# Kernel optimization log

Hardware: AMD Instinct MI355X
Metric: run time of the kernel (lower is better)

Reference implementation:

```python
import jax, jax.numpy as jnp
import numpy as np

B, SEQ, C, H, L = 2, 512, 768, 12, 6
OBS = ACT = GOAL = 64
MAXEP = 1000
D = C // H
T3 = 3 * SEQ  # stacked (z, state, action) tokens per timestep


def _ln(x, g, b):
    m = jnp.mean(x, -1, keepdims=True)
    v = jnp.mean((x - m) ** 2, -1, keepdims=True)
    return (x - m) * jax.lax.rsqrt(v + 1e-5) * g + b


def setup_inputs() -> dict:
    key = jax.random.key(0)
    it = iter(jax.random.split(key, 64))
    nrm = lambda shape, s=0.02: jax.random.normal(next(it), shape, jnp.float32) * s
    z = lambda *s: jnp.zeros(s, jnp.float32)
    o = lambda *s: jnp.ones(s, jnp.float32)
    return dict(
        states=jax.random.normal(next(it), (B, SEQ, OBS), jnp.float32),
        actions=jax.random.normal(next(it), (B, SEQ, ACT), jnp.float32),
        goals=jax.random.normal(next(it), (B, 1, GOAL), jnp.float32),
        traj_mask=jnp.ones((B, SEQ), bool),
        timesteps=jax.random.randint(next(it), (B, SEQ), 0, MAXEP),
        W_s=nrm((OBS, C)), b_s=z(C),
        W_a=nrm((ACT, C)), b_a=z(C),
        W_g=nrm((GOAL, C)), b_g=z(C),
        E_t=nrm((MAXEP, C)),
        ln0_g=o(C), ln0_b=z(C),
        Wq=nrm((L, C, C)), bq=z(L, C),
        Wk=nrm((L, C, C)), bk=z(L, C),
        Wv=nrm((L, C, C)), bv=z(L, C),
        Wp=nrm((L, C, C)), bp=z(L, C),
        ln1_g=o(L, C), ln1_b=z(L, C),
        W1=nrm((L, C, 4 * C)), b1=z(L, 4 * C),
        W2=nrm((L, 4 * C, C)), b2=z(L, C),
        ln2_g=o(L, C), ln2_b=z(L, C),
        W_ps=nrm((C, OBS)), b_ps=z(OBS),
        W_pa=nrm((C, ACT)), b_pa=z(ACT),
    )


def _forward(states, actions, goals, timesteps,
             W_s, b_s, W_a, b_a, W_g, b_g, E_t, ln0_g, ln0_b,
             Wq, bq, Wk, bk, Wv, bv, Wp, bp, ln1_g, ln1_b,
             W1, b1, W2, b2, ln2_g, ln2_b, W_ps, b_ps, W_pa, b_pa):
    te = E_t[timesteps]  # [B,SEQ,C] time embeddings (use_pe_as_timestep path)
    s_emb = states @ W_s + b_s + te
    a_emb = actions @ W_a + b_a + te
    g = jnp.broadcast_to(goals, (goals.shape[0], SEQ, goals.shape[2]))
    z_emb = g @ W_g + b_g + te  # GOAL_CONDITION path
    # interleave (z, s, a) per timestep -> [B, 3*SEQ, C]
    x = jnp.stack((z_emb, s_emb, a_emb), axis=2).reshape(states.shape[0], T3, C)
    x = _ln(x, ln0_g, ln0_b)
    mask = jnp.tril(jnp.ones((T3, T3), bool))
    scale = 1.0 / np.sqrt(D)
    for l in range(L):
        q = (x @ Wq[l] + bq[l]).reshape(-1, T3, H, D)
        k = (x @ Wk[l] + bk[l]).reshape(-1, T3, H, D)
        v = (x @ Wv[l] + bv[l]).reshape(-1, T3, H, D)
        sc = jnp.einsum('bqhd,bkhd->bhqk', q, k) * scale
        sc = jnp.where(mask, sc, -jnp.inf)
        w = jax.nn.softmax(sc, axis=-1)
        att = jnp.einsum('bhqk,bkhd->bqhd', w, v).reshape(-1, T3, C)
        x = x + att @ Wp[l] + bp[l]
        x = _ln(x, ln1_g[l], ln1_b[l])
        h = jax.nn.gelu(x @ W1[l] + b1[l], approximate=False)
        x = x + h @ W2[l] + b2[l]
        x = _ln(x, ln2_g[l], ln2_b[l])
    x = x.reshape(-1, SEQ, 3, C)
    state_preds = x[:, :, 2] @ W_ps + b_ps     # read off action-token positions
    action_preds = jnp.tanh(x[:, :, 1] @ W_pa + b_pa)  # state-token positions
    return jnp.stack((state_preds, action_preds))  # [2,B,SEQ,64]


def reference(states, actions, goals, traj_mask, timesteps,
              W_s, b_s, W_a, b_a, W_g, b_g, E_t, ln0_g, ln0_b,
              Wq, bq, Wk, bk, Wv, bv, Wp, bp, ln1_g, ln1_b,
              W1, b1, W2, b2, ln2_g, ln2_b, W_ps, b_ps, W_pa, b_pa):
    del traj_mask  # unused on the GOAL_CONDITION path
    return _forward(states, actions, goals, timesteps,
                    W_s, b_s, W_a, b_a, W_g, b_g, E_t, ln0_g, ln0_b,
                    Wq, bq, Wk, bk, Wv, bv, Wp, bp, ln1_g, ln1_b,
                    W1, b1, W2, b2, ln2_g, ln2_b, W_ps, b_ps, W_pa, b_pa)
```

## Files before the change

kernel.cpp:

```cpp
#include <hip/hip_runtime.h>

#define SEQ 512
#define T3 1536
#define CDIM 768
#define NH 12
#define HD 64
#define NL 6

typedef __attribute__((ext_vector_type(8))) short bh8;
typedef __attribute__((ext_vector_type(4))) short s4;
typedef __attribute__((ext_vector_type(4))) float f4;

__device__ inline short f2bf(float f) {
    union { float f; unsigned u; } x; x.f = f;
    unsigned r = x.u + 0x7FFFu + ((x.u >> 16) & 1u);
    return (short)(r >> 16);
}

__device__ inline void gload16(const short* g, const short* l) {
    __builtin_amdgcn_global_load_lds(
        (const __attribute__((address_space(1))) unsigned int*)g,
        (__attribute__((address_space(3))) unsigned int*)l, 16, 0, 0);
}

__device__ inline float block_sum(float v, volatile float* red, int tid) {
    #pragma unroll
    for (int off = 32; off > 0; off >>= 1) v += __shfl_down(v, off, 64);
    __syncthreads();
    if ((tid & 63) == 0) red[tid >> 6] = v;
    __syncthreads();
    return red[0] + red[1] + red[2] + red[3];
}

__global__ __launch_bounds__(256) void conv64_k(
        const float* __restrict__ Wq, const float* __restrict__ Wk,
        const float* __restrict__ Wv, const float* __restrict__ Wp,
        const float* __restrict__ W1, const float* __restrict__ W2,
        short* __restrict__ dst, int l) {
    int r = blockIdx.x;
    const float* src; short* d; int K, N, tk, tn;
    if (r < 576) {
        int mat = r / 144, t = r - mat * 144;
        tk = t / 12; tn = t % 12; K = 768; N = 768;
        const float* srcs[4] = {Wq, Wk, Wv, Wp};
        src = srcs[mat] + (size_t)l * 589824;
        d = dst + mat * 589824;
    } else if (r < 1152) {
        int t = r - 576; tk = t / 48; tn = t % 48; K = 768; N = 3072;
        src = W1 + (size_t)l * 2359296; d = dst + 2359296;
    } else {
        int t = r - 1152; tk = t / 12; tn = t % 12; K = 3072; N = 768;
        src = W2 + (size_t)l * 2359296; d = dst + 4718592;
    }
    int k0 = tk * 64, n0 = tn * 64;
    __shared__ float t2[64][65];
    int tid = threadIdx.x;
    int rk = tid >> 4, cn4 = (tid & 15) * 4;
    #pragma unroll
    for (int p = 0; p < 4; ++p) {
        f4 v = *(const f4*)(src + (size_t)(k0 + p * 16 + rk) * N + n0 + cn4);
        #pragma unroll
        for (int j = 0; j < 4; ++j) t2[cn4 + j][p * 16 + rk] = v[j];
    }
    __syncthreads();
    int n = tid >> 2, kb = (tid & 3) * 16;
    bh8 o0, o1;
    #pragma unroll
    for (int j = 0; j < 8; ++j) o0[j] = f2bf(t2[n][kb + j]);
    #pragma unroll
    for (int j = 0; j < 8; ++j) o1[j] = f2bf(t2[n][kb + 8 + j]);
    short* wp = d + (size_t)(n0 + n) * K + k0 + kb;
    *(bh8*)wp = o0;
    *(bh8*)(wp + 8) = o1;
}

__global__ __launch_bounds__(256) void embed_ln0_k(
        const float* __restrict__ states, const float* __restrict__ actions,
        const float* __restrict__ goals, const int* __restrict__ timesteps,
        const float* __restrict__ W_s, const float* __restrict__ b_s,
        const float* __restrict__ W_a, const float* __restrict__ b_a,
        const float* __restrict__ W_g, const float* __restrict__ b_g,
        const float* __restrict__ E_t, const float* __restrict__ g0,
        const float* __restrict__ bb0, float* __restrict__ x, short* __restrict__ xb) {
    int row = blockIdx.x;
    int b = row / T3, t3 = row - b * T3;
    int t = t3 / 3, kind = t3 - t * 3;
    __shared__ float inv[64];
    __shared__ float xr[CDIM];
    __shared__ float red[4];
    int tid = threadIdx.x;
    const float* src; const float* W; const float* bias;
    if (kind == 0)      { src = goals + b * 64;                       W = W_g; bias = b_g; }
    else if (kind == 1) { src = states + ((size_t)b * SEQ + t) * 64;  W = W_s; bias = b_s; }
    else                { src = actions + ((size_t)b * SEQ + t) * 64; W = W_a; bias = b_a; }
    if (tid < 64) inv[tid] = src[tid];
    __syncthreads();
    int ts = timesteps[b * SEQ + t];
    for (int c = tid; c < CDIM; c += 256) {
        float acc = bias[c] + E_t[(size_t)ts * CDIM + c];
        #pragma unroll 8
        for (int kk = 0; kk < 64; ++kk) acc += inv[kk] * W[kk * CDIM + c];
        xr[c] = acc;
    }
    __syncthreads();
    float v0 = xr[tid], v1 = xr[tid + 256], v2 = xr[tid + 512];
    float mean = block_sum(v0 + v1 + v2, red, tid) * (1.f / CDIM);
    float d0 = v0 - mean, d1 = v1 - mean, d2 = v2 - mean;
    float var = block_sum(d0 * d0 + d1 * d1 + d2 * d2, red, tid) * (1.f / CDIM);
    float rs = rsqrtf(var + 1e-5f);
    float* w = x + (size_t)row * CDIM;
    short* wb = xb + (size_t)row * CDIM;
    float o0 = d0 * rs * g0[tid]       + bb0[tid];
    float o1 = d1 * rs * g0[tid + 256] + bb0[tid + 256];
    float o2 = d2 * rs * g0[tid + 512] + bb0[tid + 512];
    w[tid] = o0; w[tid + 256] = o1; w[tid + 512] = o2;
    wb[tid] = f2bf(o0); wb[tid + 256] = f2bf(o1); wb[tid + 512] = f2bf(o2);
}

__global__ __launch_bounds__(256) void ln_k(const float* __restrict__ in, float* __restrict__ outp,
                                            short* __restrict__ outb,
                                            const float* __restrict__ g, const float* __restrict__ bb) {
    int row = blockIdx.x, tid = threadIdx.x;
    __shared__ float red[4];
    const float* r = in + (size_t)row * CDIM;
    float v0 = r[tid], v1 = r[tid + 256], v2 = r[tid + 512];
    float mean = block_sum(v0 + v1 + v2, red, tid) * (1.f / CDIM);
    float d0 = v0 - mean, d1 = v1 - mean, d2 = v2 - mean;
    float var = block_sum(d0 * d0 + d1 * d1 + d2 * d2, red, tid) * (1.f / CDIM);
    float rs = rsqrtf(var + 1e-5f);
    float* w = outp + (size_t)row * CDIM;
    short* wb = outb + (size_t)row * CDIM;
    float o0 = d0 * rs * g[tid]       + bb[tid];
    float o1 = d1 * rs * g[tid + 256] + bb[tid + 256];
    float o2 = d2 * rs * g[tid + 512] + bb[tid + 512];
    w[tid] = o0; w[tid + 256] = o1; w[tid + 512] = o2;
    wb[tid] = f2bf(o0); wb[tid + 256] = f2bf(o1); wb[tid + 512] = f2bf(o2);
}

template<int BM, int EPI>
__global__ __launch_bounds__(256) void gemm3_k(
        const short* __restrict__ A, const short* __restrict__ B0,
        const short* __restrict__ B1, const short* __restrict__ B2,
        const float* __restrict__ bias0, const float* __restrict__ bias1,
        const float* __restrict__ bias2, const float* __restrict__ res,
        float* __restrict__ outF, short* __restrict__ outQ,
        short* __restrict__ outK, short* __restrict__ outV,
        int N, int K) {
    const short* Bw = B0; const float* bias = bias0; short* outB = outQ;
    int zid = 0;
    if (EPI == 0) {
        zid = blockIdx.z;
        if (zid == 1) { Bw = B1; bias = bias1; outB = outK; }
        else if (zid == 2) { Bw = B2; bias = bias2; outB = outV; }
    }
    __shared__ short As[BM * 64];
    __shared__ short Bs[128 * 64];
    int tid = threadIdx.x, lane = tid & 63, wave = tid >> 6;
    int wm = wave >> 1, wn = wave & 1, lr = lane & 15, lg = lane >> 4;
    int bm = blockIdx.y * BM, bn = blockIdx.x * 128;
    int rl = lane >> 3, ch = (lane & 7) ^ rl;
    constexpr int MI = BM / 32;
    f4 acc[MI][4] = {};
    for (int k0 = 0; k0 < K; k0 += 64) {
        #pragma unroll
        for (int j = 0; j < BM / 32; ++j)
            gload16(A + (size_t)(bm + wave * (BM / 4) + j * 8 + rl) * K + k0 + ch * 8,
                    As + (wave * (BM / 4) + j * 8) * 64);
        #pragma unroll
        for (int j = 0; j < 4; ++j)
            gload16(Bw + (size_t)(bn + wave * 32 + j * 8 + rl) * K + k0 + ch * 8,
                    Bs + (wave * 32 + j * 8) * 64);
        __syncthreads();
        bh8 af[MI][2], bf[4][2];
        #pragma unroll
        for (int mi = 0; mi < MI; ++mi)
        #pragma unroll
        for (int kk = 0; kk < 2; ++kk) {
            int m = wm * (BM / 2) + mi * 16 + lr;
            af[mi][kk] = *(const bh8*)(As + m * 64 + (((kk * 4 + lg) ^ (lr & 7)) * 8));
        }
        #pragma unroll
        for (int ni = 0; ni < 4; ++ni)
        #pragma unroll
        for (int kk = 0; kk < 2; ++kk) {
            int n = wn * 64 + ni * 16 + lr;
            bf[ni][kk] = *(const bh8*)(Bs + n * 64 + (((kk * 4 + lg) ^ (lr & 7)) * 8));
        }
        #pragma unroll
        for (int kk = 0; kk < 2; ++kk)
        #pragma unroll
        for (int mi = 0; mi < MI; ++mi)
        #pragma unroll
        for (int ni = 0; ni < 4; ++ni)
            acc[mi][ni] = __builtin_amdgcn_mfma_f32_16x16x32_bf16(af[mi][kk], bf[ni][kk], acc[mi][ni], 0, 0, 0);
        __syncthreads();
    }
    #pragma unroll
    for (int mi = 0; mi < MI; ++mi)
    #pragma unroll
    for (int ni = 0; ni < 4; ++ni)
    #pragma unroll
    for (int i = 0; i < 4; ++i) {
        int row = bm + wm * (BM / 2) + mi * 16 + lg * 4 + i;
        int col = bn + wn * 64 + ni * 16 + lr;
        float vv = acc[mi][ni][i] + bias[col];
        if (EPI == 0) {
            int b = row / T3, t = row - b * T3;
            int h = col >> 6, d = col & 63;
            if (zid == 2) outB[((size_t)(b * NH + h) * 64 + d) * T3 + t] = f2bf(vv);
            else          outB[((((size_t)b * NH + h) * T3 + t) << 6) + d] = f2bf(vv);
        } else if (EPI == 1) {
            outF[(size_t)row * N + col] = vv + res[(size_t)row * N + col];
        } else {
            float gl = 0.5f * vv * (1.0f + erff(vv * 0.70710678118f));
            outQ[(size_t)row * N + col] = f2bf(gl);
        }
    }
}

__global__ __launch_bounds__(256) void attn_k(const short* __restrict__ q, const short* __restrict__ k,
                                              const short* __restrict__ vt, short* __restrict__ att) {
    int idx = blockIdx.x;
    int qt = 23 - (idx / 24);
    int bh = idx % 24;
    int b = bh / NH, h = bh - b * NH;
    const short* qb = q  + (size_t)bh * T3 * HD;
    const short* kb = k  + (size_t)bh * T3 * HD;
    const short* vb = vt + (size_t)bh * HD * T3;
    __shared__ short Ks[2][4096];
    __shared__ short Vs[2][4096];
    __shared__ short Pl[4][16][72];
    int tid = threadIdx.x, lane = tid & 63, wave = tid >> 6;
    int lr = lane & 15, lg = lane >> 4;
    int rl = lane >> 3, ch = (lane & 7) ^ rl;
    int qrow0 = qt * 64 + wave * 16;
    bh8 aq0 = *(const bh8*)(qb + (size_t)(qrow0 + lr) * HD + lg * 8);
    bh8 aq1 = *(const bh8*)(qb + (size_t)(qrow0 + lr) * HD + 32 + lg * 8);
    f4 o[4] = {};
    float lsum[4] = {0.f, 0.f, 0.f, 0.f};

    auto STAGE = [&](int kt2, int buf) {
        const short* kb2 = kb + (size_t)kt2 * 64 * HD;
        #pragma unroll
        for (int j = 0; j < 2; ++j)
            gload16(kb2 + (wave * 16 + j * 8 + rl) * HD + ch * 8,
                    &Ks[buf][(wave * 16 + j * 8) * 64]);
        const short* vb2 = vb + kt2 * 64;
        #pragma unroll
        for (int j = 0; j < 2; ++j)
            gload16(vb2 + (size_t)(wave * 16 + j * 8 + rl) * T3 + ch * 8,
                    &Vs[buf][(wave * 16 + j * 8) * 64]);
    };

    STAGE(0, 0);
    int cur = 0;
    for (int kt = 0; kt <= qt; ++kt) {
        if (kt < qt) {
            STAGE(kt + 1, cur ^ 1);
            asm volatile("s_waitcnt vmcnt(4)" ::: "memory");
        } else {
            asm volatile("s_waitcnt vmcnt(0)" ::: "memory");
        }
        __builtin_amdgcn_s_barrier();
        __builtin_amdgcn_sched_barrier(0);
        const short* Kb = &Ks[cur][0];
        const short* Vb = &Vs[cur][0];
        f4 s[4];
        #pragma unroll
        for (int nf = 0; nf < 4; ++nf) {
            int tok = nf * 16 + lr;
            bh8 bk0 = *(const bh8*)(Kb + tok * 64 + ((lg ^ (lr & 7)) * 8));
            bh8 bk1 = *(const bh8*)(Kb + tok * 64 + (((4 + lg) ^ (lr & 7)) * 8));
            f4 t = {};
            t = __builtin_amdgcn_mfma_f32_16x16x32_bf16(aq0, bk0, t, 0, 0, 0);
            t = __builtin_amdgcn_mfma_f32_16x16x32_bf16(aq1, bk1, t, 0, 0, 0);
            s[nf] = t;
        }
        #pragma unroll
        for (int nf = 0; nf < 4; ++nf)
        #pragma unroll
        for (int i = 0; i < 4; ++i) {
            float p = __expf(s[nf][i] * 0.125f);
            if (kt == qt && (nf * 16 + lr) > (wave * 16 + lg * 4 + i)) p = 0.f;
            lsum[i] += p;
            Pl[wave][lg * 4 + i][nf * 16 + lr] = f2bf(p);
        }
        bh8 ap0 = *(const bh8*)&Pl[wave][lr][lg * 8];
        bh8 ap1 = *(const bh8*)&Pl[wave][lr][32 + lg * 8];
        #pragma unroll
        for (int nf = 0; nf < 4; ++nf) {
            int d = nf * 16 + lr;
            bh8 bv0 = *(const bh8*)(Vb + d * 64 + ((lg ^ (lr & 7)) * 8));
            bh8 bv1 = *(const bh8*)(Vb + d * 64 + (((4 + lg) ^ (lr & 7)) * 8));
            o[nf] = __builtin_amdgcn_mfma_f32_16x16x32_bf16(ap0, bv0, o[nf], 0, 0, 0);
            o[nf] = __builtin_amdgcn_mfma_f32_16x16x32_bf16(ap1, bv1, o[nf], 0, 0, 0);
        }
        __builtin_amdgcn_sched_barrier(0);
        __builtin_amdgcn_s_barrier();
        cur ^= 1;
    }
    float linv[4];
    #pragma unroll
    for (int i = 0; i < 4; ++i) {
        float l = lsum[i];
        #pragma unroll
        for (int off = 1; off < 16; off <<= 1) l += __shfl_xor(l, off, 16);
        linv[i] = 1.f / l;
    }
    #pragma unroll
    for (int nf = 0; nf < 4; ++nf)
    #pragma unroll
    for (int i = 0; i < 4; ++i) {
        int qrow = qrow0 + lg * 4 + i;
        att[((size_t)b * T3 + qrow) * CDIM + h * 64 + nf * 16 + lr] = f2bf(o[nf][i] * linv[i]);
    }
}

__global__ __launch_bounds__(64) void head_k(const float* __restrict__ x,
                                             const float* __restrict__ Wps, const float* __restrict__ bps,
                                             const float* __restrict__ Wpa, const float* __restrict__ bpa,
                                             float* __restrict__ out) {
    int o = blockIdx.y;
    int bs = blockIdx.x;
    int b = bs >> 9, t = bs & 511;
    int kind = (o == 0) ? 2 : 1;
    const float* W = (o == 0) ? Wps : Wpa;
    const float* bi = (o == 0) ? bps : bpa;
    const float* xr = x + ((size_t)b * T3 + t * 3 + kind) * CDIM;
    int n = threadIdx.x;
    float a0 = 0.f, a1 = 0.f, a2 = 0.f, a3 = 0.f;
    for (int kk = 0; kk < CDIM; kk += 4) {
        a0 = fmaf(xr[kk],     W[(kk)     * 64 + n], a0);
        a1 = fmaf(xr[kk + 1], W[(kk + 1) * 64 + n], a1);
        a2 = fmaf(xr[kk + 2], W[(kk + 2) * 64 + n], a2);
        a3 = fmaf(xr[kk + 3], W[(kk + 3) * 64 + n], a3);
    }
    float acc = bi[n] + ((a0 + a1) + (a2 + a3));
    if (o == 1) acc = tanhf(acc);
    out[(((size_t)o * 2 + b) * SEQ + t) * 64 + n] = acc;
}

extern "C" void kernel_launch(void* const* d_in, const int* in_sizes, int n_in,
                              void* d_out, int out_size, void* d_ws, size_t ws_size,
                              hipStream_t stream) {
    const float* states    = (const float*)d_in[0];
    const float* actions   = (const float*)d_in[1];
    const float* goals     = (const float*)d_in[2];
    const int*   timesteps = (const int*)d_in[4];
    const float* W_s = (const float*)d_in[5];  const float* b_s = (const float*)d_in[6];
    const float* W_a = (const float*)d_in[7];  const float* b_a = (const float*)d_in[8];
    const float* W_g = (const float*)d_in[9];  const float* b_g = (const float*)d_in[10];
    const float* E_t = (const float*)d_in[11];
    const float* ln0_g = (const float*)d_in[12]; const float* ln0_b = (const float*)d_in[13];
    const float* Wq = (const float*)d_in[14]; const float* bq = (const float*)d_in[15];
    const float* Wk = (const float*)d_in[16]; const float* bk = (const float*)d_in[17];
    const float* Wv = (const float*)d_in[18]; const float* bv = (const float*)d_in[19];
    const float* Wp = (const float*)d_in[20]; const float* bp = (const float*)d_in[21];
    const float* ln1_g = (const float*)d_in[22]; const float* ln1_b = (const float*)d_in[23];
    const float* W1 = (const float*)d_in[24]; const float* b1 = (const float*)d_in[25];
    const float* W2 = (const float*)d_in[26]; const float* b2 = (const float*)d_in[27];
    const float* ln2_g = (const float*)d_in[28]; const float* ln2_b = (const float*)d_in[29];
    const float* W_ps = (const float*)d_in[30]; const float* b_ps = (const float*)d_in[31];
    const float* W_pa = (const float*)d_in[32]; const float* b_pa = (const float*)d_in[33];

    char* ws = (char*)d_ws;
    float* x_f   = (float*)(ws);
    float* x2_f  = (float*)(ws + 9437184);
    short* x_bf  = (short*)(ws + 18874368);
    short* attb  = (short*)(ws + 23592960);
    short* h_bf  = (short*)(ws + 28311552);
    short* qb    = (short*)(ws + 47185920);
    short* kb    = (short*)(ws + 51904512);
    short* vbt   = (short*)(ws + 56623104);
    short* wts   = (short*)(ws + 61341696);

    embed_ln0_k<<<dim3(2 * T3), 256, 0, stream>>>(states, actions, goals, timesteps,
        W_s, b_s, W_a, b_a, W_g, b_g, E_t, ln0_g, ln0_b, x_f, x_bf);

    for (int l = 0; l < NL; ++l) {
        size_t bo = (size_t)l * CDIM, b1o = (size_t)l * 4 * CDIM;
        conv64_k<<<dim3(1728), 256, 0, stream>>>(Wq, Wk, Wv, Wp, W1, W2, wts, l);
        short* Wqt = wts;
        short* Wkt = wts + 589824;
        short* Wvt = wts + 1179648;
        short* Wpt = wts + 1769472;
        short* W1t = wts + 2359296;
        short* W2t = wts + 4718592;

        gemm3_k<128, 0><<<dim3(6, 24, 3), 256, 0, stream>>>(x_bf, Wqt, Wkt, Wvt,
            bq + bo, bk + bo, bv + bo, nullptr, nullptr, qb, kb, vbt, CDIM, CDIM);
        attn_k<<<dim3(576), 256, 0, stream>>>(qb, kb, vbt, attb);
        gemm3_k<64, 1><<<dim3(6, 48, 1), 256, 0, stream>>>(attb, Wpt, nullptr, nullptr,
            bp + bo, nullptr, nullptr, x_f, x2_f, nullptr, nullptr, nullptr, CDIM, CDIM);
        ln_k<<<dim3(2 * T3), 256, 0, stream>>>(x2_f, x_f, x_bf, ln1_g + bo, ln1_b + bo);
        gemm3_k<128, 2><<<dim3(24, 24, 1), 256, 0, stream>>>(x_bf, W1t, nullptr, nullptr,
            b1 + b1o, nullptr, nullptr, nullptr, nullptr, h_bf, nullptr, nullptr, 4 * CDIM, CDIM);
        gemm3_k<64, 1><<<dim3(6, 48, 1), 256, 0, stream>>>(h_bf, W2t, nullptr, nullptr,
            b2 + bo, nullptr, nullptr, x_f, x2_f, nullptr, nullptr, nullptr, CDIM, 4 * CDIM);
        ln_k<<<dim3(2 * T3), 256, 0, stream>>>(x2_f, x_f, x_bf, ln2_g + bo, ln2_b + bo);
    }

    head_k<<<dim3(1024, 2), 64, 0, stream>>>(x_f, W_ps, b_ps, W_pa, b_pa, (float*)d_out);
}
```

Measured before the change: 1.176 ms.

## Double-buffer GEMM loads, batch weight conversion, and apply residual and LayerNorm in place

The GEMM main loop now double-buffers its A and B tiles in LDS, using partial vmcnt waits and raw barriers so the next tile's global loads overlap the current MFMAs. Weight conversion for all six layers runs in one launch when the workspace is large enough, replacing six per-layer launches. The residual add and LayerNorm now work in place on x_f, removing the x2_f buffer, and attention writes into x_bf. The head reads the bf16 activations, which costs a little precision. Together these aim to cut memory traffic, launch count, and load stalls inside the GEMMs.

```diff
diff --git a/kernel.cpp b/kernel.cpp
--- a/kernel.cpp
+++ b/kernel.cpp
@@ -17,6 +17,12 @@
     return (short)(r >> 16);
 }
 
+__device__ inline float bf2f(short s) {
+    union { unsigned u; float f; } x;
+    x.u = ((unsigned)(unsigned short)s) << 16;
+    return x.f;
+}
+
 __device__ inline void gload16(const short* g, const short* l) {
     __builtin_amdgcn_global_load_lds(
         (const __attribute__((address_space(1))) unsigned int*)g,
@@ -36,21 +42,24 @@
         const float* __restrict__ Wq, const float* __restrict__ Wk,
         const float* __restrict__ Wv, const float* __restrict__ Wp,
         const float* __restrict__ W1, const float* __restrict__ W2,
-        short* __restrict__ dst, int l) {
-    int r = blockIdx.x;
+        short* __restrict__ dst, int l0) {
+    int flat = blockIdx.x;
+    int lrel = flat / 1728, r = flat - lrel * 1728;
+    int l = l0 + lrel;
+    short* dstL = dst + (size_t)lrel * 7077888;
     const float* src; short* d; int K, N, tk, tn;
     if (r < 576) {
         int mat = r / 144, t = r - mat * 144;
         tk = t / 12; tn = t % 12; K = 768; N = 768;
         const float* srcs[4] = {Wq, Wk, Wv, Wp};
         src = srcs[mat] + (size_t)l * 589824;
-        d = dst + mat * 589824;
+        d = dstL + mat * 589824;
     } else if (r < 1152) {
         int t = r - 576; tk = t / 48; tn = t % 48; K = 768; N = 3072;
-        src = W1 + (size_t)l * 2359296; d = dst + 2359296;
+        src = W1 + (size_t)l * 2359296; d = dstL + 2359296;
     } else {
         int t = r - 1152; tk = t / 12; tn = t % 12; K = 3072; N = 768;
-        src = W2 + (size_t)l * 2359296; d = dst + 4718592;
+        src = W2 + (size_t)l * 2359296; d = dstL + 4718592;
     }
     int k0 = tk * 64, n0 = tn * 64;
     __shared__ float t2[64][65];
@@ -117,32 +126,30 @@
     wb[tid] = f2bf(o0); wb[tid + 256] = f2bf(o1); wb[tid + 512] = f2bf(o2);
 }
 
-__global__ __launch_bounds__(256) void ln_k(const float* __restrict__ in, float* __restrict__ outp,
-                                            short* __restrict__ outb,
+__global__ __launch_bounds__(256) void ln_k(float* __restrict__ x, short* __restrict__ outb,
                                             const float* __restrict__ g, const float* __restrict__ bb) {
     int row = blockIdx.x, tid = threadIdx.x;
     __shared__ float red[4];
-    const float* r = in + (size_t)row * CDIM;
+    float* r = x + (size_t)row * CDIM;
     float v0 = r[tid], v1 = r[tid + 256], v2 = r[tid + 512];
     float mean = block_sum(v0 + v1 + v2, red, tid) * (1.f / CDIM);
     float d0 = v0 - mean, d1 = v1 - mean, d2 = v2 - mean;
     float var = block_sum(d0 * d0 + d1 * d1 + d2 * d2, red, tid) * (1.f / CDIM);
     float rs = rsqrtf(var + 1e-5f);
-    float* w = outp + (size_t)row * CDIM;
     short* wb = outb + (size_t)row * CDIM;
     float o0 = d0 * rs * g[tid]       + bb[tid];
     float o1 = d1 * rs * g[tid + 256] + bb[tid + 256];
     float o2 = d2 * rs * g[tid + 512] + bb[tid + 512];
-    w[tid] = o0; w[tid + 256] = o1; w[tid + 512] = o2;
+    r[tid] = o0; r[tid + 256] = o1; r[tid + 512] = o2;
     wb[tid] = f2bf(o0); wb[tid + 256] = f2bf(o1); wb[tid + 512] = f2bf(o2);
 }
 
 template<int BM, int EPI>
-__global__ __launch_bounds__(256) void gemm3_k(
+__global__ __launch_bounds__(256) void gemm4_k(
         const short* __restrict__ A, const short* __restrict__ B0,
         const short* __restrict__ B1, const short* __restrict__ B2,
         const float* __restrict__ bias0, const float* __restrict__ bias1,
-        const float* __restrict__ bias2, const float* __restrict__ res,
+        const float* __restrict__ bias2,
         float* __restrict__ outF, short* __restrict__ outQ,
         short* __restrict__ outK, short* __restrict__ outV,
         int N, int K) {
@@ -153,38 +160,52 @@
         if (zid == 1) { Bw = B1; bias = bias1; outB = outK; }
         else if (zid == 2) { Bw = B2; bias = bias2; outB = outV; }
     }
-    __shared__ short As[BM * 64];
-    __shared__ short Bs[128 * 64];
+    __shared__ short As[2][BM * 64];
+    __shared__ short Bs[2][128 * 64];
     int tid = threadIdx.x, lane = tid & 63, wave = tid >> 6;
     int wm = wave >> 1, wn = wave & 1, lr = lane & 15, lg = lane >> 4;
     int bm = blockIdx.y * BM, bn = blockIdx.x * 128;
     int rl = lane >> 3, ch = (lane & 7) ^ rl;
     constexpr int MI = BM / 32;
-    f4 acc[MI][4] = {};
-    for (int k0 = 0; k0 < K; k0 += 64) {
+
+    auto STAGE = [&](int k0, int buf) {
         #pragma unroll
         for (int j = 0; j < BM / 32; ++j)
             gload16(A + (size_t)(bm + wave * (BM / 4) + j * 8 + rl) * K + k0 + ch * 8,
-                    As + (wave * (BM / 4) + j * 8) * 64);
+                    &As[buf][(wave * (BM / 4) + j * 8) * 64]);
         #pragma unroll
         for (int j = 0; j < 4; ++j)
             gload16(Bw + (size_t)(bn + wave * 32 + j * 8 + rl) * K + k0 + ch * 8,
-                    Bs + (wave * 32 + j * 8) * 64);
-        __syncthreads();
+                    &Bs[buf][(wave * 32 + j * 8) * 64]);
+    };
+
+    f4 acc[MI][4] = {};
+    STAGE(0, 0);
+    int cur = 0;
+    for (int k0 = 0; k0 < K; k0 += 64) {
+        if (k0 + 64 < K) {
+            STAGE(k0 + 64, cur ^ 1);
+            if constexpr (BM == 128) asm volatile("s_waitcnt vmcnt(8)" ::: "memory");
+            else                     asm volatile("s_waitcnt vmcnt(6)" ::: "memory");
+        } else {
+            asm volatile("s_waitcnt vmcnt(0)" ::: "memory");
+        }
+        __builtin_amdgcn_s_barrier();
+        __builtin_amdgcn_sched_barrier(0);
         bh8 af[MI][2], bf[4][2];
         #pragma unroll
         for (int mi = 0; mi < MI; ++mi)
         #pragma unroll
         for (int kk = 0; kk < 2; ++kk) {
             int m = wm * (BM / 2) + mi * 16 + lr;
-            af[mi][kk] = *(const bh8*)(As + m * 64 + (((kk * 4 + lg) ^ (lr & 7)) * 8));
+            af[mi][kk] = *(const bh8*)(&As[cur][m * 64 + (((kk * 4 + lg) ^ (lr & 7)) * 8)]);
         }
         #pragma unroll
         for (int ni = 0; ni < 4; ++ni)
         #pragma unroll
         for (int kk = 0; kk < 2; ++kk) {
             int n = wn * 64 + ni * 16 + lr;
-            bf[ni][kk] = *(const bh8*)(Bs + n * 64 + (((kk * 4 + lg) ^ (lr & 7)) * 8));
+            bf[ni][kk] = *(const bh8*)(&Bs[cur][n * 64 + (((kk * 4 + lg) ^ (lr & 7)) * 8)]);
         }
         #pragma unroll
         for (int kk = 0; kk < 2; ++kk)
@@ -193,7 +214,9 @@
         #pragma unroll
         for (int ni = 0; ni < 4; ++ni)
             acc[mi][ni] = __builtin_amdgcn_mfma_f32_16x16x32_bf16(af[mi][kk], bf[ni][kk], acc[mi][ni], 0, 0, 0);
-        __syncthreads();
+        __builtin_amdgcn_sched_barrier(0);
+        __builtin_amdgcn_s_barrier();
+        cur ^= 1;
     }
     #pragma unroll
     for (int mi = 0; mi < MI; ++mi)
@@ -210,7 +233,8 @@
             if (zid == 2) outB[((size_t)(b * NH + h) * 64 + d) * T3 + t] = f2bf(vv);
             else          outB[((((size_t)b * NH + h) * T3 + t) << 6) + d] = f2bf(vv);
         } else if (EPI == 1) {
-            outF[(size_t)row * N + col] = vv + res[(size_t)row * N + col];
+            size_t idx = (size_t)row * N + col;
+            outF[idx] = vv + outF[idx];
         } else {
             float gl = 0.5f * vv * (1.0f + erff(vv * 0.70710678118f));
             outQ[(size_t)row * N + col] = f2bf(gl);
@@ -316,7 +340,7 @@
     }
 }
 
-__global__ __launch_bounds__(64) void head_k(const float* __restrict__ x,
+__global__ __launch_bounds__(64) void head_k(const short* __restrict__ x,
                                              const float* __restrict__ Wps, const float* __restrict__ bps,
                                              const float* __restrict__ Wpa, const float* __restrict__ bpa,
                                              float* __restrict__ out) {
@@ -326,14 +350,15 @@
     int kind = (o == 0) ? 2 : 1;
     const float* W = (o == 0) ? Wps : Wpa;
     const float* bi = (o == 0) ? bps : bpa;
-    const float* xr = x + ((size_t)b * T3 + t * 3 + kind) * CDIM;
+    const short* xr = x + ((size_t)b * T3 + t * 3 + kind) * CDIM;
     int n = threadIdx.x;
     float a0 = 0.f, a1 = 0.f, a2 = 0.f, a3 = 0.f;
     for (int kk = 0; kk < CDIM; kk += 4) {
-        a0 = fmaf(xr[kk],     W[(kk)     * 64 + n], a0);
-        a1 = fmaf(xr[kk + 1], W[(kk + 1) * 64 + n], a1);
-        a2 = fmaf(xr[kk + 2], W[(kk + 2) * 64 + n], a2);
-        a3 = fmaf(xr[kk + 3], W[(kk + 3) * 64 + n], a3);
+        s4 xv = *(const s4*)(xr + kk);
+        a0 = fmaf(bf2f(xv[0]), W[(kk)     * 64 + n], a0);
+        a1 = fmaf(bf2f(xv[1]), W[(kk + 1) * 64 + n], a1);
+        a2 = fmaf(bf2f(xv[2]), W[(kk + 2) * 64 + n], a2);
+        a3 = fmaf(bf2f(xv[3]), W[(kk + 3) * 64 + n], a3);
     }
     float acc = bi[n] + ((a0 + a1) + (a2 + a3));
     if (o == 1) acc = tanhf(acc);
@@ -365,40 +390,46 @@
 
     char* ws = (char*)d_ws;
     float* x_f   = (float*)(ws);
-    float* x2_f  = (float*)(ws + 9437184);
-    short* x_bf  = (short*)(ws + 18874368);
-    short* attb  = (short*)(ws + 23592960);
-    short* h_bf  = (short*)(ws + 28311552);
-    short* qb    = (short*)(ws + 47185920);
-    short* kb    = (short*)(ws + 51904512);
-    short* vbt   = (short*)(ws + 56623104);
-    short* wts   = (short*)(ws + 61341696);
+    short* x_bf  = (short*)(ws + 9437184);
+    short* h_bf  = (short*)(ws + 14155776);
+    short* qb    = (short*)(ws + 33030144);
+    short* kb    = (short*)(ws + 37748736);
+    short* vbt   = (short*)(ws + 42467328);
+    short* wts   = (short*)(ws + 47185920);
+
+    const long long WL = 7077888;
+    bool allw = ws_size >= 132120576ull;
 
     embed_ln0_k<<<dim3(2 * T3), 256, 0, stream>>>(states, actions, goals, timesteps,
         W_s, b_s, W_a, b_a, W_g, b_g, E_t, ln0_g, ln0_b, x_f, x_bf);
 
+    if (allw)
+        conv64_k<<<dim3(1728 * NL), 256, 0, stream>>>(Wq, Wk, Wv, Wp, W1, W2, wts, 0);
+
     for (int l = 0; l < NL; ++l) {
         size_t bo = (size_t)l * CDIM, b1o = (size_t)l * 4 * CDIM;
-        conv64_k<<<dim3(1728), 256, 0, stream>>>(Wq, Wk, Wv, Wp, W1, W2, wts, l);
-        short* Wqt = wts;
-        short* Wkt = wts + 589824;
-        short* Wvt = wts + 1179648;
-        short* Wpt = wts + 1769472;
-        short* W1t = wts + 2359296;
-        short* W2t = wts + 4718592;
-
-        gemm3_k<128, 0><<<dim3(6, 24, 3), 256, 0, stream>>>(x_bf, Wqt, Wkt, Wvt,
-            bq + bo, bk + bo, bv + bo, nullptr, nullptr, qb, kb, vbt, CDIM, CDIM);
-        attn_k<<<dim3(576), 256, 0, stream>>>(qb, kb, vbt, attb);
-        gemm3_k<64, 1><<<dim3(6, 48, 1), 256, 0, stream>>>(attb, Wpt, nullptr, nullptr,
-            bp + bo, nullptr, nullptr, x_f, x2_f, nullptr, nullptr, nullptr, CDIM, CDIM);
-        ln_k<<<dim3(2 * T3), 256, 0, stream>>>(x2_f, x_f, x_bf, ln1_g + bo, ln1_b + bo);
-        gemm3_k<128, 2><<<dim3(24, 24, 1), 256, 0, stream>>>(x_bf, W1t, nullptr, nullptr,
-            b1 + b1o, nullptr, nullptr, nullptr, nullptr, h_bf, nullptr, nullptr, 4 * CDIM, CDIM);
-        gemm3_k<64, 1><<<dim3(6, 48, 1), 256, 0, stream>>>(h_bf, W2t, nullptr, nullptr,
-            b2 + bo, nullptr, nullptr, x_f, x2_f, nullptr, nullptr, nullptr, CDIM, 4 * CDIM);
-        ln_k<<<dim3(2 * T3), 256, 0, stream>>>(x2_f, x_f, x_bf, ln2_g + bo, ln2_b + bo);
-    }
-
-    head_k<<<dim3(1024, 2), 64, 0, stream>>>(x_f, W_ps, b_ps, W_pa, b_pa, (float*)d_out);
-}
+        if (!allw)
+            conv64_k<<<dim3(1728), 256, 0, stream>>>(Wq, Wk, Wv, Wp, W1, W2, wts, l);
+        short* wb  = wts + (allw ? (long long)l * WL : 0);
+        short* Wqt = wb;
+        short* Wkt = wb + 589824;
+        short* Wvt = wb + 1179648;
+        short* Wpt = wb + 1769472;
+        short* W1t = wb + 2359296;
+        short* W2t = wb + 4718592;
+
+        gemm4_k<128, 0><<<dim3(6, 24, 3), 256, 0, stream>>>(x_bf, Wqt, Wkt, Wvt,
+            bq + bo, bk + bo, bv + bo, nullptr, qb, kb, vbt, CDIM, CDIM);
+        attn_k<<<dim3(576), 256, 0, stream>>>(qb, kb, vbt, x_bf);
+        gemm4_k<64, 1><<<dim3(6, 48, 1), 256, 0, stream>>>(x_bf, Wpt, nullptr, nullptr,
+            bp + bo, nullptr, nullptr, x_f, nullptr, nullptr, nullptr, CDIM, CDIM);
+        ln_k<<<dim3(2 * T3), 256, 0, stream>>>(x_f, x_bf, ln1_g + bo, ln1_b + bo);
+        gemm4_k<128, 2><<<dim3(24, 24, 1), 256, 0, stream>>>(x_bf, W1t, nullptr, nullptr,
+            b1 + b1o, nullptr, nullptr, nullptr, h_bf, nullptr, nullptr, 4 * CDIM, CDIM);
+        gemm4_k<64, 1><<<dim3(6, 48, 1), 256, 0, stream>>>(h_bf, W2t, nullptr, nullptr,
+            b2 + bo, nullptr, nullptr, x_f, nullptr, nullptr, nullptr, CDIM, 4 * CDIM);
+        ln_k<<<dim3(2 * T3), 256, 0, stream>>>(x_f, x_bf, ln2_g + bo, ln2_b + bo);
+    }
+
+    head_k<<<dim3(1024, 2), 64, 0, stream>>>(x_bf, W_ps, b_ps, W_pa, b_pa, (float*)d_out);
+}
```

Measured after the change: 1.216 ms. 1.03x slower.
